# Performance work log

Hardware: AMD Instinct MI355X
Metric: run time of the kernel (lower is better)

## Reference

```python
import jax, jax.numpy as jnp
import numpy as np

K = 3          # kernel_size
PAD = 1
STRIDE = 1
GF = 1.5       # grad_factor (affects backward only)

# Each of the 16 difflogic gates g(a,b) is affine in {1, a, b, a*b}:
# columns = [const, coef_a, coef_b, coef_ab]
GATE_M = jnp.array([
    [0, 0, 0, 0],   # 0: False
    [0, 0, 0, 1],   # 1: a AND b
    [0, 1, 0, -1],  # 2: a AND NOT b
    [0, 1, 0, 0],   # 3: a
    [0, 0, 1, -1],  # 4: NOT a AND b
    [0, 0, 1, 0],   # 5: b
    [0, 1, 1, -2],  # 6: XOR
    [0, 1, 1, -1],  # 7: OR
    [1, -1, -1, 1], # 8: NOR
    [1, -1, -1, 2], # 9: XNOR
    [1, 0, -1, 0],  # 10: NOT b
    [1, 0, -1, 1],  # 11: a OR NOT b
    [1, -1, 0, 0],  # 12: NOT a
    [1, -1, 0, 1],  # 13: NOT a OR b
    [1, 0, 0, -1],  # 14: NAND
    [1, 0, 0, 0],   # 15: True
], dtype=jnp.float32)

B, C, H, W = 32, 32, 32, 32
O = 64  # out_channels
LAYER_DIMS = [(288, 32), (32, 16), (16, 8), (8, 4), (4, 2), (2, 1)]


def setup_inputs() -> dict:
    key = jax.random.key(0)
    ks = jax.random.split(key, 1 + 3 * len(LAYER_DIMS))
    inp = {"x": jax.random.uniform(ks[0], (B, C, H, W), dtype=jnp.float32)}
    for l, (di, do) in enumerate(LAYER_DIMS):
        inp[f"ia{l}"] = jax.random.randint(ks[1 + 3 * l], (O, do), 0, di, dtype=jnp.int32)
        inp[f"ib{l}"] = jax.random.randint(ks[2 + 3 * l], (O, do), 0, di, dtype=jnp.int32)
        w = 0.1 * jax.random.normal(ks[3 + 3 * l], (O, do, 16), dtype=jnp.float32)
        inp[f"w{l}"] = w.at[:, :, 3].add(5.0)  # 'residual' init: bias pass-through gate
    return inp


def _grad_scale(x):
    # difflogic GradFactor: identity in value, scales grads by GF in backward
    return x * GF - jax.lax.stop_gradient(x) * (GF - 1.0)


def _logic_layer(x, ia, ib, w):
    # x: [N, in] (shared layer-0 input) or [N, O, in]; ia/ib: [O, out]; w: [O, out, 16]
    x = _grad_scale(x)
    if x.ndim == 2:
        a = x[:, ia]            # [N, O, out]
        b = x[:, ib]
    else:
        oidx = jnp.arange(x.shape[1])[:, None]  # [O, 1]
        a = x[:, oidx, ia]      # per-filter gather -> [N, O, out]
        b = x[:, oidx, ib]
    coef = jax.nn.softmax(w, axis=-1) @ GATE_M  # [O, out, 4]
    return coef[..., 0] + coef[..., 1] * a + coef[..., 2] * b + coef[..., 3] * (a * b)


def _extract_patches(x):
    # faithful to F.unfold: channel-major [B, C*K*K, L] patch layout
    b, c, h, w = x.shape
    xp = jnp.pad(x, ((0, 0), (0, 0), (PAD, PAD), (PAD, PAD)))
    oh = (h + 2 * PAD - K) // STRIDE + 1
    ow = (w + 2 * PAD - K) // STRIDE + 1
    pats = jnp.stack([xp[:, :, ki:ki + oh * STRIDE:STRIDE, kj:kj + ow * STRIDE:STRIDE]
                      for ki in range(K) for kj in range(K)], axis=2)  # [B, C, K*K, oh, ow]
    pats = pats.reshape(b, c * K * K, oh * ow)        # [B, C*K*K, L]
    pats = pats.transpose(0, 2, 1).reshape(b * oh * ow, c * K * K)  # [(B L), C*K*K]
    return pats, oh, ow


def _forward(x, ws, ias, ibs):
    b = x.shape[0]
    pats, oh, ow = _extract_patches(x)
    h = pats  # [N, in_dim], shared across all O filters
    for w_l, ia_l, ib_l in zip(ws, ias, ibs):
        h = _logic_layer(h, ia_l, ib_l, w_l)  # -> [N, O, out_l]
    y = h[..., 0]                              # [N, O]
    y = y.reshape(b, oh * ow, O).transpose(0, 2, 1).reshape(b, O, oh, ow)
    return y


def reference(x, ia0, ib0, ia1, ib1, ia2, ib2, ia3, ib3, ia4, ib4, ia5, ib5,
              w0, w1, w2, w3, w4, w5):
    ws = (w0, w1, w2, w3, w4, w5)
    ias = (ia0, ia1, ia2, ia3, ia4, ia5)
    ibs = (ib0, ib1, ib2, ib3, ib4, ib5)
    return _forward(x, ws, ias, ibs)
```

## Files before the change

kernel.cpp:

```cpp
#include <hip/hip_runtime.h>
#include <math.h>


struct Tabs { const int* ia[6]; const int* ib[6]; const float* w[6]; };

__device__ __constant__ float GM[64] = {
  0,0,0,0,   0,0,0,1,   0,1,0,-1,  0,1,0,0,
  0,0,1,-1,  0,0,1,0,   0,1,1,-2,  0,1,1,-1,
  1,-1,-1,1, 1,-1,-1,2, 1,0,-1,0,  1,0,-1,1,
  1,-1,0,0,  1,-1,0,1,  1,0,0,-1,  1,0,0,0 };

typedef float v2f __attribute__((ext_vector_type(2)));

__device__ __forceinline__ v2f gatep(v2f a, v2f b, float4 c) {
  v2f t = __builtin_elementwise_fma((v2f)c.w, b, (v2f)c.y);
  t = __builtin_elementwise_fma(a, t, (v2f)c.x);
  return __builtin_elementwise_fma((v2f)c.z, b, t);
}

__global__ __launch_bounds__(256) void build_tree(Tabs t, unsigned* __restrict tab) {
  const int gid = blockIdx.x * 256 + threadIdx.x;
  const int o = gid >> 6, slot = gid & 63;
  if (slot >= 63) return;
  int L, m;
  if      (slot < 32) { L = 0; m = slot;      }
  else if (slot < 48) { L = 1; m = slot - 32; }
  else if (slot < 56) { L = 2; m = slot - 48; }
  else if (slot < 60) { L = 3; m = slot - 56; }
  else if (slot < 62) { L = 4; m = slot - 60; }
  else                { L = 5; m = 0;         }
  const int dcnt[6] = {32, 16, 8, 4, 2, 1};
  const int d = 5 - L;
  int g = 0;
  for (int step = 0; step < d; ++step) {
    int lyr = 5 - step;
    int bit = (m >> (d - 1 - step)) & 1;
    g = (bit ? t.ib[lyr] : t.ia[lyr])[o * dcnt[lyr] + g];
  }

  const float4* wp = (const float4*)(t.w[L] + (o * dcnt[L] + g) * 16);
  float4 w0 = wp[0], w1 = wp[1], w2 = wp[2], w3 = wp[3];
  float wv[16] = { w0.x,w0.y,w0.z,w0.w, w1.x,w1.y,w1.z,w1.w,
                   w2.x,w2.y,w2.z,w2.w, w3.x,w3.y,w3.z,w3.w };
  float mx = -1e30f;
  #pragma unroll
  for (int k = 0; k < 16; ++k) mx = fmaxf(mx, wv[k]);
  float e[16], s = 0.f;
  #pragma unroll
  for (int k = 0; k < 16; ++k) { e[k] = expf(wv[k] - mx); s += e[k]; }
  float inv = 1.0f / s;
  float c0 = 0, c1 = 0, c2 = 0, c3 = 0;
  #pragma unroll
  for (int k = 0; k < 16; ++k) {
    float p = e[k] * inv;
    c0 += p * GM[k*4+0]; c1 += p * GM[k*4+1];
    c2 += p * GM[k*4+2]; c3 += p * GM[k*4+3];
  }
  float4* C = (float4*)(tab + o * 288 + 32);
  float4 c; c.x = c0; c.y = c1; c.z = c2; c.w = c3;
  C[slot] = c;

  if (L == 0) {
    int ia = t.ia[0][o * 32 + g], ib = t.ib[0][o * 32 + g];
    int ca = ia / 9, ra = ia - ca * 9, kia = ra / 3, kja = ra - kia * 3;
    int cb = ib / 9, rb = ib - cb * 9, kib = rb / 3, kjb = rb - kib * 3;
    unsigned offa = (unsigned)((ca * 6 + kia) * 35 + kja);
    unsigned offb = (unsigned)((cb * 6 + kib) * 35 + kjb);
    tab[o * 288 + slot] = offa | (offb << 16);
  }
}

__global__ __launch_bounds__(512, 8) void logic_conv(const float* __restrict x,
                                                     const unsigned* __restrict tab,
                                                     float* __restrict out) {
  __shared__ float xr[6720];
  const int bid = blockIdx.x;
  const int tc = bid & 3, rc = (bid >> 2) & 7, b = bid >> 5;
  const int r0 = rc * 4;
  const int tid = threadIdx.x;

  for (int idx = tid; idx < 6720; idx += 512) {
    int c = idx / 210, rem = idx - c * 210;
    int rr = rem / 35, sc = rem - rr * 35;
    int gr = r0 - 1 + rr, gc = sc - 1;
    float v = 0.f;
    if ((unsigned)gr < 32u && (unsigned)gc < 32u)
      v = x[((b * 32 + c) * 32 + gr) * 32 + gc];
    xr[idx] = v;
  }
  __syncthreads();

  const int w = tid >> 6;
  const int lane = tid & 63;
  const int rbase = lane >> 4;
  const int j = (lane & 15) * 2;
  const int lbase = rbase * 35 + j;
  const int o0 = tc * 16 + w * 2;
  float* outb = out + ((b * 64 + o0) * 32 + (r0 + rbase)) * 32 + j;

  for (int t = 0; t < 2; ++t) {
    const int o = __builtin_amdgcn_readfirstlane(o0 + t);
    const unsigned* __restrict T = tab + o * 288;
    const float4*  __restrict C = (const float4*)(T + 32);

    v2f t1[16];
    #pragma unroll
    for (int n = 0; n < 16; ++n) {
      unsigned ipA = T[2*n], ipB = T[2*n+1];
      int oa = (int)(ipA & 0xffffu) + lbase;
      int ob = (int)(ipA >> 16) + lbase;
      v2f a, bb;
      a.x = xr[oa]; a.y = xr[oa + 1];
      bb.x = xr[ob]; bb.y = xr[ob + 1];
      v2f u = gatep(a, bb, C[2*n]);
      oa = (int)(ipB & 0xffffu) + lbase;
      ob = (int)(ipB >> 16) + lbase;
      v2f cc, dd;
      cc.x = xr[oa]; cc.y = xr[oa + 1];
      dd.x = xr[ob]; dd.y = xr[ob + 1];
      v2f v = gatep(cc, dd, C[2*n+1]);
      t1[n] = gatep(u, v, C[32 + n]);
    }
    v2f t2[8];
    #pragma unroll
    for (int n = 0; n < 8; ++n) t2[n] = gatep(t1[2*n], t1[2*n+1], C[48 + n]);
    v2f t3[4];
    #pragma unroll
    for (int n = 0; n < 4; ++n) t3[n] = gatep(t2[2*n], t2[2*n+1], C[56 + n]);
    v2f t4[2];
    #pragma unroll
    for (int n = 0; n < 2; ++n) t4[n] = gatep(t3[2*n], t3[2*n+1], C[60 + n]);
    {
      v2f r = gatep(t4[0], t4[1], C[62]);
      float2 rr; rr.x = r.x; rr.y = r.y;
      *(float2*)outb = rr;
    }
    outb += 1024;
  }
}

extern "C" void kernel_launch(void* const* d_in, const int* in_sizes, int n_in,
                              void* d_out, int out_size, void* d_ws, size_t ws_size,
                              hipStream_t stream) {
  const float* x = (const float*)d_in[0];
  Tabs tabs;
  for (int l = 0; l < 6; ++l) {
    tabs.ia[l] = (const int*)d_in[1 + 3 * l];
    tabs.ib[l] = (const int*)d_in[2 + 3 * l];
    tabs.w[l]  = (const float*)d_in[3 + 3 * l];
  }
  unsigned* tab = (unsigned*)d_ws;
  build_tree<<<16, 256, 0, stream>>>(tabs, tab);
  logic_conv<<<1024, 512, 0, stream>>>(x, tab, (float*)d_out);
}
```

Baseline: 28.80 us.

## Stage input tile as packed fp16 pairs with even/odd-shifted LDS copies

The shared-memory input tile now holds pairs of adjacent pixels as packed half2 words. Two copies are stored, one aligned to even columns and one shifted by one column, so each thread fetches both of its output pixels with a single 32-bit LDS read instead of two float reads. The offset table is re-encoded to point into the correct copy. This halves the LDS load instructions in the hot loop but adds fp16 conversions and rounds the inputs to half precision, which may affect accuracy.

```diff
diff --git a/kernel.cpp b/kernel.cpp
--- a/kernel.cpp
+++ b/kernel.cpp
@@ -1,4 +1,5 @@
 #include <hip/hip_runtime.h>
+#include <hip/hip_fp16.h>
 #include <math.h>
 
 
@@ -64,39 +65,50 @@
     int ia = t.ia[0][o * 32 + g], ib = t.ib[0][o * 32 + g];
     int ca = ia / 9, ra = ia - ca * 9, kia = ra / 3, kja = ra - kia * 3;
     int cb = ib / 9, rb = ib - cb * 9, kib = rb / 3, kjb = rb - kib * 3;
-    unsigned offa = (unsigned)((ca * 6 + kia) * 35 + kja);
-    unsigned offb = (unsigned)((cb * 6 + kib) * 35 + kjb);
-    tab[o * 288 + slot] = offa | (offb << 16);
+    int hA = (ca * 6 + kia) * 48 + kja;
+    int hB = (cb * 6 + kib) * 48 + kjb;
+    unsigned dwa = (hA & 1) ? (unsigned)(((hA - 1) >> 1) + 4608) : (unsigned)(hA >> 1);
+    unsigned dwb = (hB & 1) ? (unsigned)(((hB - 1) >> 1) + 4608) : (unsigned)(hB >> 1);
+    tab[o * 288 + slot] = dwa | (dwb << 16);
   }
 }
 
 __global__ __launch_bounds__(512, 8) void logic_conv(const float* __restrict x,
                                                      const unsigned* __restrict tab,
                                                      float* __restrict out) {
-  __shared__ float xr[6720];
+  __shared__ unsigned xr[9216];
   const int bid = blockIdx.x;
   const int tc = bid & 3, rc = (bid >> 2) & 7, b = bid >> 5;
   const int r0 = rc * 4;
   const int tid = threadIdx.x;
 
-  for (int idx = tid; idx < 6720; idx += 512) {
-    int c = idx / 210, rem = idx - c * 210;
-    int rr = rem / 35, sc = rem - rr * 35;
-    int gr = r0 - 1 + rr, gc = sc - 1;
-    float v = 0.f;
-    if ((unsigned)gr < 32u && (unsigned)gc < 32u)
-      v = x[((b * 32 + c) * 32 + gr) * 32 + gc];
-    xr[idx] = v;
+  for (int k = tid; k < 4608; k += 512) {
+    int ch = k / 144, rem = k - ch * 144;
+    int rr = rem / 24, kk = rem - rr * 24;
+    int gr = r0 - 1 + rr;
+    int gc = 2 * kk - 1;
+    float fm = 0.f, f0 = 0.f, fp = 0.f;
+    if ((unsigned)gr < 32u) {
+      const float* base = x + ((b * 32 + ch) * 32 + gr) * 32;
+      if ((unsigned)gc < 32u)       fm = base[gc];
+      if ((unsigned)(gc + 1) < 32u) f0 = base[gc + 1];
+      if ((unsigned)(gc + 2) < 32u) fp = base[gc + 2];
+    }
+    unsigned hm = __half_as_ushort(__float2half(fm));
+    unsigned h0 = __half_as_ushort(__float2half(f0));
+    unsigned hp = __half_as_ushort(__float2half(fp));
+    xr[k]        = hm | (h0 << 16);
+    xr[k + 4608] = h0 | (hp << 16);
   }
   __syncthreads();
 
   const int w = tid >> 6;
   const int lane = tid & 63;
   const int rbase = lane >> 4;
-  const int j = (lane & 15) * 2;
-  const int lbase = rbase * 35 + j;
+  const int jh = lane & 15;
+  const int ldw = rbase * 24 + jh;
   const int o0 = tc * 16 + w * 2;
-  float* outb = out + ((b * 64 + o0) * 32 + (r0 + rbase)) * 32 + j;
+  float* outb = out + ((b * 64 + o0) * 32 + (r0 + rbase)) * 32 + 2 * jh;
 
   for (int t = 0; t < 2; ++t) {
     const int o = __builtin_amdgcn_readfirstlane(o0 + t);
@@ -107,18 +119,18 @@
     #pragma unroll
     for (int n = 0; n < 16; ++n) {
       unsigned ipA = T[2*n], ipB = T[2*n+1];
-      int oa = (int)(ipA & 0xffffu) + lbase;
-      int ob = (int)(ipA >> 16) + lbase;
-      v2f a, bb;
-      a.x = xr[oa]; a.y = xr[oa + 1];
-      bb.x = xr[ob]; bb.y = xr[ob + 1];
+      unsigned da = xr[(int)(ipA & 0xffffu) + ldw];
+      unsigned db = xr[(int)(ipA >> 16) + ldw];
+      float2 fa = __half22float2(*reinterpret_cast<__half2*>(&da));
+      float2 fb = __half22float2(*reinterpret_cast<__half2*>(&db));
+      v2f a = {fa.x, fa.y}, bb = {fb.x, fb.y};
       v2f u = gatep(a, bb, C[2*n]);
-      oa = (int)(ipB & 0xffffu) + lbase;
-      ob = (int)(ipB >> 16) + lbase;
-      v2f cc, dd;
-      cc.x = xr[oa]; cc.y = xr[oa + 1];
-      dd.x = xr[ob]; dd.y = xr[ob + 1];
-      v2f v = gatep(cc, dd, C[2*n+1]);
+      unsigned dc = xr[(int)(ipB & 0xffffu) + ldw];
+      unsigned dd = xr[(int)(ipB >> 16) + ldw];
+      float2 fc = __half22float2(*reinterpret_cast<__half2*>(&dc));
+      float2 fd = __half22float2(*reinterpret_cast<__half2*>(&dd));
+      v2f cc = {fc.x, fc.y}, ddv = {fd.x, fd.y};
+      v2f v = gatep(cc, ddv, C[2*n+1]);
       t1[n] = gatep(u, v, C[32 + n]);
     }
     v2f t2[8];
```

New measurement: 32.07 us. +11.4%, slower.

## Fetch half of layer-0 operands from a padded global copy instead of LDS

Applied to the files above, without the earlier changes.

Adds a prep kernel that writes a padded, column-rearranged copy of x into workspace, and a new conv kernel that reads the b operand of each first-layer gate from that global copy through precomputed offsets. The a operands still come from LDS. The intent is to halve LDS read traffic by moving half of it onto the vector-memory/L2 path. In exchange it adds an extra kernel launch, writes and reads a buffer of roughly 10 MB, and adds global load latency inside the inner loop. The original LDS-only kernel is kept as a fallback when the workspace is too small.

```diff
diff --git a/kernel.cpp b/kernel.cpp
--- a/kernel.cpp
+++ b/kernel.cpp
@@ -3,6 +3,10 @@
 
 
 struct Tabs { const int* ia[6]; const int* ib[6]; const float* w[6]; };
+
+#define TAB_STRIDE 320
+#define XP_OFF_DW  20480
+#define XP_DWORDS  2506752
 
 __device__ __constant__ float GM[64] = {
   0,0,0,0,   0,0,0,1,   0,1,0,-1,  0,1,0,0,
@@ -56,7 +60,7 @@
     c0 += p * GM[k*4+0]; c1 += p * GM[k*4+1];
     c2 += p * GM[k*4+2]; c3 += p * GM[k*4+3];
   }
-  float4* C = (float4*)(tab + o * 288 + 32);
+  float4* C = (float4*)(tab + o * TAB_STRIDE + 32);
   float4 c; c.x = c0; c.y = c1; c.z = c2; c.w = c3;
   C[slot] = c;
 
@@ -66,13 +70,32 @@
     int cb = ib / 9, rb = ib - cb * 9, kib = rb / 3, kjb = rb - kib * 3;
     unsigned offa = (unsigned)((ca * 6 + kia) * 35 + kja);
     unsigned offb = (unsigned)((cb * 6 + kib) * 35 + kjb);
-    tab[o * 288 + slot] = offa | (offb << 16);
-  }
-}
-
-__global__ __launch_bounds__(512, 8) void logic_conv(const float* __restrict x,
-                                                     const unsigned* __restrict tab,
-                                                     float* __restrict out) {
+    tab[o * TAB_STRIDE + slot] = offa | (offb << 16);
+    unsigned inrow = (kjb == 1) ? 38u : (unsigned)kjb;
+    tab[o * TAB_STRIDE + 288 + slot] = (unsigned)(cb * 2448 + kib * 72) + inrow;
+  }
+}
+
+__global__ __launch_bounds__(256) void prep(const float* __restrict x,
+                                            float* __restrict xp) {
+  int idx = blockIdx.x * 256 + threadIdx.x;
+  if (idx >= XP_DWORDS) return;
+  int i = idx % 72;
+  int rowid = idx / 72;
+  int r = rowid % 34;
+  int bc = rowid / 34;
+  int col = (i < 36) ? (i - 1) : (i - 38);
+  int gr = r - 1;
+  float v = 0.f;
+  if ((unsigned)gr < 32u && (unsigned)col < 32u)
+    v = x[(bc * 32 + gr) * 32 + col];
+  xp[idx] = v;
+}
+
+__global__ __launch_bounds__(512, 8) void logic_conv_g(const float* __restrict x,
+                                                       const unsigned* __restrict tab,
+                                                       const float* __restrict xp,
+                                                       float* __restrict out) {
   __shared__ float xr[6720];
   const int bid = blockIdx.x;
   const int tc = bid & 3, rc = (bid >> 2) & 7, b = bid >> 5;
@@ -96,11 +119,81 @@
   const int j = (lane & 15) * 2;
   const int lbase = rbase * 35 + j;
   const int o0 = tc * 16 + w * 2;
+  const int blg = b * 78336 + (r0 + rbase) * 72 + j;
+  const float* __restrict xpl = xp + blg;
   float* outb = out + ((b * 64 + o0) * 32 + (r0 + rbase)) * 32 + j;
 
   for (int t = 0; t < 2; ++t) {
     const int o = __builtin_amdgcn_readfirstlane(o0 + t);
-    const unsigned* __restrict T = tab + o * 288;
+    const unsigned* __restrict T  = tab + o * TAB_STRIDE;
+    const float4*  __restrict C  = (const float4*)(T + 32);
+    const unsigned* __restrict G2 = T + 288;
+
+    v2f t1[16];
+    #pragma unroll
+    for (int n = 0; n < 16; ++n) {
+      unsigned ipA = T[2*n], ipB = T[2*n+1];
+      int oa = (int)(ipA & 0xffffu) + lbase;
+      v2f a; a.x = xr[oa]; a.y = xr[oa + 1];
+      float2 fb = *(const float2*)(xpl + (int)G2[2*n]);
+      v2f bb = {fb.x, fb.y};
+      v2f u = gatep(a, bb, C[2*n]);
+      int oc = (int)(ipB & 0xffffu) + lbase;
+      v2f cc; cc.x = xr[oc]; cc.y = xr[oc + 1];
+      float2 fd = *(const float2*)(xpl + (int)G2[2*n+1]);
+      v2f dd = {fd.x, fd.y};
+      v2f v = gatep(cc, dd, C[2*n+1]);
+      t1[n] = gatep(u, v, C[32 + n]);
+    }
+    v2f t2[8];
+    #pragma unroll
+    for (int n = 0; n < 8; ++n) t2[n] = gatep(t1[2*n], t1[2*n+1], C[48 + n]);
+    v2f t3[4];
+    #pragma unroll
+    for (int n = 0; n < 4; ++n) t3[n] = gatep(t2[2*n], t2[2*n+1], C[56 + n]);
+    v2f t4[2];
+    #pragma unroll
+    for (int n = 0; n < 2; ++n) t4[n] = gatep(t3[2*n], t3[2*n+1], C[60 + n]);
+    {
+      v2f r = gatep(t4[0], t4[1], C[62]);
+      float2 rr; rr.x = r.x; rr.y = r.y;
+      *(float2*)outb = rr;
+    }
+    outb += 1024;
+  }
+}
+
+__global__ __launch_bounds__(512, 8) void logic_conv_r(const float* __restrict x,
+                                                       const unsigned* __restrict tab,
+                                                       float* __restrict out) {
+  __shared__ float xr[6720];
+  const int bid = blockIdx.x;
+  const int tc = bid & 3, rc = (bid >> 2) & 7, b = bid >> 5;
+  const int r0 = rc * 4;
+  const int tid = threadIdx.x;
+
+  for (int idx = tid; idx < 6720; idx += 512) {
+    int c = idx / 210, rem = idx - c * 210;
+    int rr = rem / 35, sc = rem - rr * 35;
+    int gr = r0 - 1 + rr, gc = sc - 1;
+    float v = 0.f;
+    if ((unsigned)gr < 32u && (unsigned)gc < 32u)
+      v = x[((b * 32 + c) * 32 + gr) * 32 + gc];
+    xr[idx] = v;
+  }
+  __syncthreads();
+
+  const int w = tid >> 6;
+  const int lane = tid & 63;
+  const int rbase = lane >> 4;
+  const int j = (lane & 15) * 2;
+  const int lbase = rbase * 35 + j;
+  const int o0 = tc * 16 + w * 2;
+  float* outb = out + ((b * 64 + o0) * 32 + (r0 + rbase)) * 32 + j;
+
+  for (int t = 0; t < 2; ++t) {
+    const int o = __builtin_amdgcn_readfirstlane(o0 + t);
+    const unsigned* __restrict T = tab + o * TAB_STRIDE;
     const float4*  __restrict C = (const float4*)(T + 32);
 
     v2f t1[16];
@@ -151,5 +244,13 @@
   }
   unsigned* tab = (unsigned*)d_ws;
   build_tree<<<16, 256, 0, stream>>>(tabs, tab);
-  logic_conv<<<1024, 512, 0, stream>>>(x, tab, (float*)d_out);
-}
+
+  const size_t need = (size_t)(XP_OFF_DW + XP_DWORDS) * 4;
+  if (ws_size >= need) {
+    float* xp = (float*)d_ws + XP_OFF_DW;
+    prep<<<(XP_DWORDS + 255) / 256, 256, 0, stream>>>(x, xp);
+    logic_conv_g<<<1024, 512, 0, stream>>>(x, tab, xp, (float*)d_out);
+  } else {
+    logic_conv_r<<<1024, 512, 0, stream>>>(x, tab, (float*)d_out);
+  }
+}
```

New measurement: 45.74 us. +58.8%, slower.
